# Kernel tuning notes

Measured on AMD Instinct MI355X. Metric: run time of the kernel, lower is better.

## Reference

```python
import jax, jax.numpy as jnp
import numpy as np

D = 7            # tree max depth (n_locations = 4**D = 16384)
M = 128          # memory_dim
N_KEYS = sum(4 ** i for i in range(1, D + 1))      # 21844
N_INTERNAL = N_KEYS // 4                           # 5461


def setup_inputs() -> dict:
    key = jax.random.key(0)
    ks = jax.random.split(key, 6)
    B, C = 4096, 64
    hidden = jax.random.normal(ks[0], (B, C), dtype=jnp.float32)
    Wq = jax.random.normal(ks[1], (M, C), dtype=jnp.float32) * 0.05
    bq = jnp.zeros((M,), dtype=jnp.float32)
    states = jax.random.normal(ks[2], (N_KEYS, M), dtype=jnp.float32)
    Wk = jax.random.normal(ks[3], (D, M, M), dtype=jnp.float32) * 0.05
    bk = jnp.zeros((D, M), dtype=jnp.float32)
    return {"hidden": hidden, "Wq": Wq, "bq": bq, "states": states, "Wk": Wk, "bk": bk}


def reference(hidden, Wq, bq, states, Wk, bk):
    B = hidden.shape[0]
    # hidden_to_query (pre-training path uses class_to_query): [B, M]
    query = hidden @ Wq.T + bq
    # make_keys: per-depth state_to_key linear + activation on batch-independent states
    keys = []
    cursor = 0
    for i in range(D):
        n = 4 ** (i + 1)
        keys.append(jax.nn.relu(states[cursor:cursor + n] @ Wk[i].T + bk[i]))
        cursor += n
    keys = jnp.concatenate(keys, axis=0)               # [N_KEYS, M]
    # compute_scores: bmm(keys, query^T) -> [B, N_INTERNAL, 4]
    scores = jnp.einsum('km,bm->bk', keys, query).reshape(B, N_INTERNAL, 4)
    # to_location_distribution (is_consistent, pre_training): cumulative log-softmax down the tree
    logp = jax.nn.log_softmax(scores, axis=-1)         # [B, N_INTERNAL, 4]
    dists = []
    cur = None
    cursor = 0
    for d in range(1, D + 1):
        n_parents = 4 ** (d - 1)
        layer = logp[:, cursor:cursor + n_parents, :].reshape(B, 4 ** d)
        cur = layer if cur is None else jnp.repeat(cur, 4, axis=-1) + layer
        dists.append(cur)                              # [B, 4**d]
        cursor += n_parents
    return tuple(dists)
```

## Files before the change

### kernel.cpp

```cpp
#include <hip/hip_runtime.h>
#include <hip/hip_bf16.h>
#include <math.h>

#define MDIM 128
#define CDIM 64
#define NTILES 1366

typedef __attribute__((ext_vector_type(8))) __bf16 bf16x8;
typedef __attribute__((ext_vector_type(4))) float f32x4;

__global__ __launch_bounds__(256) void k_cvtw(const float* __restrict__ Wk,
                                              __hip_bfloat16* __restrict__ wkb) {
  const int i = blockIdx.x * 256 + threadIdx.x;
  float4 v = *reinterpret_cast<const float4*>(Wk + (size_t)i * 4);
  __hip_bfloat16 h[4];
  h[0] = __float2bfloat16(v.x); h[1] = __float2bfloat16(v.y);
  h[2] = __float2bfloat16(v.z); h[3] = __float2bfloat16(v.w);
  unsigned long long bits;
  __builtin_memcpy(&bits, h, 8);
  *reinterpret_cast<unsigned long long*>(wkb + (size_t)i * 4) = bits;
}

#define STR 144

__global__ __launch_bounds__(64) void k_keys_mfma(const float* __restrict__ states,
                                                  const __hip_bfloat16* __restrict__ wkb,
                                                  const float* __restrict__ bk,
                                                  bf16x8* __restrict__ keysF) {
  __shared__ __align__(16) __hip_bfloat16 sT[16 * STR];
  const int lane = threadIdx.x;
  const int c = lane & 15, hi = lane >> 4;
  int blk = blockIdx.x, d, t;
  if      (blk < 2)   { d = blk; t = 0; }
  else if (blk < 6)   { d = 2; t = blk - 2; }
  else if (blk < 22)  { d = 3; t = blk - 6; }
  else if (blk < 86)  { d = 4; t = blk - 22; }
  else if (blk < 342) { d = 5; t = blk - 86; }
  else                { d = 6; t = blk - 342; }
  const int cumArr[7] = {0, 4, 20, 84, 340, 1364, 5460};
  const int k0 = cumArr[d] + 16 * t;

  bf16x8 sb[4];
  const float* srow = states + (size_t)(k0 + c) * MDIM;
#pragma unroll
  for (int kf = 0; kf < 4; ++kf) {
    float4 a = *reinterpret_cast<const float4*>(srow + kf * 32 + hi * 8);
    float4 b = *reinterpret_cast<const float4*>(srow + kf * 32 + hi * 8 + 4);
    bf16x8 v;
    v[0] = (__bf16)a.x; v[1] = (__bf16)a.y; v[2] = (__bf16)a.z; v[3] = (__bf16)a.w;
    v[4] = (__bf16)b.x; v[5] = (__bf16)b.y; v[6] = (__bf16)b.z; v[7] = (__bf16)b.w;
    sb[kf] = v;
  }

  const __hip_bfloat16* wkd = wkb + (size_t)d * MDIM * MDIM;
  const float* bkd = bk + d * MDIM;

#pragma unroll
  for (int ct = 0; ct < 8; ++ct) {
    bf16x8 aw[4];
    const __hip_bfloat16* wrow = wkd + (size_t)(ct * 16 + c) * MDIM;
#pragma unroll
    for (int kf = 0; kf < 4; ++kf)
      aw[kf] = *reinterpret_cast<const bf16x8*>(wrow + kf * 32 + hi * 8);
    f32x4 acc = {};
#pragma unroll
    for (int kf = 0; kf < 4; ++kf)
      acc = __builtin_amdgcn_mfma_f32_16x16x32_bf16(aw[kf], sb[kf], acc, 0, 0, 0);
    float4 bias = *reinterpret_cast<const float4*>(bkd + ct * 16 + hi * 4);
    __hip_bfloat16 hv[4];
    hv[0] = __float2bfloat16(fmaxf(acc[0] + bias.x, 0.f));
    hv[1] = __float2bfloat16(fmaxf(acc[1] + bias.y, 0.f));
    hv[2] = __float2bfloat16(fmaxf(acc[2] + bias.z, 0.f));
    hv[3] = __float2bfloat16(fmaxf(acc[3] + bias.w, 0.f));
    unsigned long long bits;
    __builtin_memcpy(&bits, hv, 8);
    *reinterpret_cast<unsigned long long*>(&sT[c * STR + ct * 16 + 4 * hi]) = bits;
  }

#pragma unroll
  for (int kf = 0; kf < 4; ++kf) {
    bf16x8 v = *reinterpret_cast<const bf16x8*>(&sT[c * STR + kf * 32 + hi * 8]);
    keysF[(size_t)(blk * 4 + kf) * 64 + lane] = v;
  }
}

__global__ __launch_bounds__(128) void k_query(const float* __restrict__ hidden,
                                               const float* __restrict__ Wq,
                                               const float* __restrict__ bq,
                                               __hip_bfloat16* __restrict__ query) {
  __shared__ __align__(16) float sH[4][CDIM];
  const int b0 = blockIdx.x * 4;
  const int m  = threadIdx.x;
  for (int idx = m; idx < 4 * CDIM; idx += 128)
    sH[idx >> 6][idx & 63] = hidden[(size_t)b0 * CDIM + idx];
  __syncthreads();
  const float4* wrow = (const float4*)(Wq + (size_t)m * CDIM);
  float acc0 = 0.f, acc1 = 0.f, acc2 = 0.f, acc3 = 0.f;
#pragma unroll
  for (int kq = 0; kq < CDIM / 4; ++kq) {
    float4 w = wrow[kq];
    float4 a = *(const float4*)&sH[0][kq * 4];
    float4 b = *(const float4*)&sH[1][kq * 4];
    float4 c = *(const float4*)&sH[2][kq * 4];
    float4 e = *(const float4*)&sH[3][kq * 4];
    acc0 += w.x * a.x + w.y * a.y + w.z * a.z + w.w * a.w;
    acc1 += w.x * b.x + w.y * b.y + w.z * b.z + w.w * b.w;
    acc2 += w.x * c.x + w.y * c.y + w.z * c.z + w.w * c.w;
    acc3 += w.x * e.x + w.y * e.y + w.z * e.z + w.w * e.w;
  }
  const float bias = bq[m];
  query[(size_t)(b0 + 0) * MDIM + m] = __float2bfloat16(acc0 + bias);
  query[(size_t)(b0 + 1) * MDIM + m] = __float2bfloat16(acc1 + bias);
  query[(size_t)(b0 + 2) * MDIM + m] = __float2bfloat16(acc2 + bias);
  query[(size_t)(b0 + 3) * MDIM + m] = __float2bfloat16(acc3 + bias);
}

#define D7STR 68

struct Frag { bf16x8 f[4]; };

__device__ __forceinline__ void load_frags(const bf16x8* __restrict__ kF,
                                           int blk, Frag& fr, int lane) {
#pragma unroll
  for (int kf = 0; kf < 4; ++kf)
    fr.f[kf] = kF[(size_t)(blk * 4 + kf) * 64 + lane];
}

__device__ __forceinline__ float gather_par(const f32x4 cp, int u, int lane) {
  const int src = u * 16 + (lane & 15);
  const float g0 = __shfl(cp[0], src, 64);
  const float g1 = __shfl(cp[1], src, 64);
  const float g2 = __shfl(cp[2], src, 64);
  const float g3 = __shfl(cp[3], src, 64);
  const int hi = lane >> 4;
  const float p01 = (hi & 1) ? g1 : g0;
  const float p23 = (hi & 1) ? g3 : g2;
  return (hi & 2) ? p23 : p01;
}

__device__ __forceinline__ void tile_step(
    const bf16x8* __restrict__ kF, const Frag& cur, int nextBlk, Frag& nxt,
    const bf16x8 (&qf)[4], const f32x4* cumPrev, int u, f32x4& cumOut,
    float* __restrict__ oPtr, size_t span, bool doStore, bool d1mask,
    float* __restrict__ d7dst, int lane) {
  const int c = lane & 15, hi = lane >> 4;

  if (nextBlk >= 0) load_frags(kF, nextBlk, nxt, lane);

  f32x4 acc = {};
  acc = __builtin_amdgcn_mfma_f32_16x16x32_bf16(cur.f[0], qf[0], acc, 0, 0, 0);
  acc = __builtin_amdgcn_mfma_f32_16x16x32_bf16(cur.f[1], qf[1], acc, 0, 0, 0);
  acc = __builtin_amdgcn_mfma_f32_16x16x32_bf16(cur.f[2], qf[2], acc, 0, 0, 0);
  acc = __builtin_amdgcn_mfma_f32_16x16x32_bf16(cur.f[3], qf[3], acc, 0, 0, 0);

  const float lse = __logf(__expf(acc[0]) + __expf(acc[1]) +
                           __expf(acc[2]) + __expf(acc[3]));
  float par = 0.f;
  if (cumPrev) par = gather_par(*cumPrev, u, lane);
  f32x4 cm;
  cm[0] = acc[0] - lse + par;
  cm[1] = acc[1] - lse + par;
  cm[2] = acc[2] - lse + par;
  cm[3] = acc[3] - lse + par;
  cumOut = cm;

  if (d7dst) {
    *reinterpret_cast<f32x4*>(d7dst + c * D7STR) = cm;
  } else if (doStore && (!d1mask || hi == 0)) {
    float4 o;
    o.x = cm[0]; o.y = cm[1]; o.z = cm[2]; o.w = cm[3];
    *reinterpret_cast<float4*>(oPtr + (size_t)c * span + hi * 4) = o;
  }
}

__global__ __launch_bounds__(256) void k_tree(const bf16x8* __restrict__ kF,
                                              const __hip_bfloat16* __restrict__ query,
                                              float* __restrict__ out, int B) {
  __shared__ __align__(16) float sD7[4][16 * D7STR];

  const int tid  = threadIdx.x;
  const int lane = tid & 63;
  const int w    = tid >> 6;
  const int c    = lane & 15, hi = lane >> 4;

  const int S5  = blockIdx.x & 63;
  const int bg  = blockIdx.x >> 6;
  const int T4  = S5 >> 2;
  const int T3  = S5 >> 4;
  const int b0w = bg * 64 + w * 16;

  float* d7w = &sD7[w][0];

  bf16x8 qf[4];
  {
    const __hip_bfloat16* qrow = query + (size_t)(b0w + c) * MDIM;
#pragma unroll
    for (int kf = 0; kf < 4; ++kf)
      qf[kf] = *reinterpret_cast<const bf16x8*>(qrow + kf * 32 + hi * 8);
  }

  Frag fA, fB;
  load_frags(kF, 0, fA, lane);

  f32x4 c1, c2, c3, c4, c5, c6, c7;

  tile_step(kF, fA, 1, fB, qf, nullptr, 0, c1,
            out + (size_t)b0w * 4, 4, S5 == 0, true, nullptr, lane);
  tile_step(kF, fB, 2 + T3, fA, qf, &c1, 0, c2,
            out + (size_t)4 * B + (size_t)b0w * 16, 16, S5 == 0, false,
            nullptr, lane);
  tile_step(kF, fA, 6 + T4, fB, qf, &c2, T3, c3,
            out + (size_t)20 * B + (size_t)b0w * 64 + 16 * T3, 64,
            (S5 & 15) == 0, false, nullptr, lane);
  tile_step(kF, fB, 22 + S5, fA, qf, &c3, T4 & 3, c4,
            out + (size_t)84 * B + (size_t)b0w * 256 + 16 * T4, 256,
            (S5 & 3) == 0, false, nullptr, lane);
  tile_step(kF, fA, 86 + 4 * S5, fB, qf, &c4, S5 & 3, c5,
            out + (size_t)340 * B + (size_t)b0w * 1024 + 16 * S5, 1024,
            true, false, nullptr, lane);

#pragma unroll
  for (int u5p = 0; u5p < 2; ++u5p) {
#pragma unroll
    for (int half = 0; half < 2; ++half) {
      const int u5 = u5p * 2 + half;
      Frag& f0 = (half == 0) ? fB : fA;
      Frag& f1 = (half == 0) ? fA : fB;
      const int T6 = 4 * S5 + u5;
      const int d7b = 342 + 16 * S5 + 4 * u5;
      tile_step(kF, f0, d7b, f1, qf, &c5, u5, c6,
                out + (size_t)1364 * B + (size_t)b0w * 4096 + 16 * T6, 4096,
                true, false, nullptr, lane);
      tile_step(kF, f1, d7b + 1, f0, qf, &c6, 0, c7,
                nullptr, 0, false, false, d7w + 0 * 16 + hi * 4, lane);
      tile_step(kF, f0, d7b + 2, f1, qf, &c6, 1, c7,
                nullptr, 0, false, false, d7w + 1 * 16 + hi * 4, lane);
      tile_step(kF, f1, d7b + 3, f0, qf, &c6, 2, c7,
                nullptr, 0, false, false, d7w + 2 * 16 + hi * 4, lane);
      tile_step(kF, f0, (u5 < 3) ? (86 + 4 * S5 + u5 + 1) : -1, f1, qf, &c6, 3, c7,
                nullptr, 0, false, false, d7w + 3 * 16 + hi * 4, lane);
      {
        float* dst = out + (size_t)5460 * B + (size_t)b0w * 16384 + 64 * T6;
#pragma unroll
        for (int j = 0; j < 4; ++j) {
          const int r = j * 4 + hi;
          f32x4 v = *reinterpret_cast<const f32x4*>(d7w + r * D7STR + c * 4);
          float4 o;
          o.x = v[0]; o.y = v[1]; o.z = v[2]; o.w = v[3];
          *reinterpret_cast<float4*>(dst + (size_t)r * 16384 + c * 4) = o;
        }
      }
    }
  }
}

extern "C" void kernel_launch(void* const* d_in, const int* in_sizes, int n_in,
                              void* d_out, int out_size, void* d_ws, size_t ws_size,
                              hipStream_t stream) {
  const float* hidden = (const float*)d_in[0];
  const float* Wq     = (const float*)d_in[1];
  const float* bq     = (const float*)d_in[2];
  const float* states = (const float*)d_in[3];
  const float* Wk     = (const float*)d_in[4];
  const float* bk     = (const float*)d_in[5];
  float* out = (float*)d_out;
  const int B = in_sizes[0] / CDIM;

  __hip_bfloat16* base  = (__hip_bfloat16*)d_ws;
  bf16x8* keysF = (bf16x8*)base;
  __hip_bfloat16* query = base + (size_t)NTILES * 4 * 64 * 8;
  __hip_bfloat16* wkb   = query + (size_t)B * MDIM;

  k_cvtw<<<(7 * MDIM * MDIM) / (256 * 4), 256, 0, stream>>>(Wk, wkb);
  k_query<<<B / 4, 128, 0, stream>>>(hidden, Wq, bq, query);
  k_keys_mfma<<<NTILES, 64, 0, stream>>>(states, wkb, bk, keysF);

  k_tree<<<(B / 64) * 64, 256, 0, stream>>>(keysF, query, out, B);
}
```

Measured before the change: 122.8 us.

## Process two 16-row batch tiles per wave to reuse key fragments

Each wave now handles 32 batch rows (two 16-row tiles) instead of 16, reusing every loaded key fragment for two sets of MFMAs. The grid is halved and the shared depth-7 staging buffer doubled. The aim is to halve key-fragment global loads and per-tile overhead per batch row, at the cost of more registers (two query fragment sets and two cumulative vectors per level), which may lower occupancy and gives fewer blocks to spread across CUs.

Measured after the change: 119.4 us. 2.7% less time.

```diff
diff --git a/kernel.cpp b/kernel.cpp
--- a/kernel.cpp
+++ b/kernel.cpp
@@ -140,43 +140,46 @@
 
 __device__ __forceinline__ void tile_step(
     const bf16x8* __restrict__ kF, const Frag& cur, int nextBlk, Frag& nxt,
-    const bf16x8 (&qf)[4], const f32x4* cumPrev, int u, f32x4& cumOut,
+    const bf16x8 (&qf)[2][4], const f32x4* cumPrev, int u, f32x4 (&cumOut)[2],
     float* __restrict__ oPtr, size_t span, bool doStore, bool d1mask,
     float* __restrict__ d7dst, int lane) {
   const int c = lane & 15, hi = lane >> 4;
 
   if (nextBlk >= 0) load_frags(kF, nextBlk, nxt, lane);
 
-  f32x4 acc = {};
-  acc = __builtin_amdgcn_mfma_f32_16x16x32_bf16(cur.f[0], qf[0], acc, 0, 0, 0);
-  acc = __builtin_amdgcn_mfma_f32_16x16x32_bf16(cur.f[1], qf[1], acc, 0, 0, 0);
-  acc = __builtin_amdgcn_mfma_f32_16x16x32_bf16(cur.f[2], qf[2], acc, 0, 0, 0);
-  acc = __builtin_amdgcn_mfma_f32_16x16x32_bf16(cur.f[3], qf[3], acc, 0, 0, 0);
-
-  const float lse = __logf(__expf(acc[0]) + __expf(acc[1]) +
-                           __expf(acc[2]) + __expf(acc[3]));
-  float par = 0.f;
-  if (cumPrev) par = gather_par(*cumPrev, u, lane);
-  f32x4 cm;
-  cm[0] = acc[0] - lse + par;
-  cm[1] = acc[1] - lse + par;
-  cm[2] = acc[2] - lse + par;
-  cm[3] = acc[3] - lse + par;
-  cumOut = cm;
-
-  if (d7dst) {
-    *reinterpret_cast<f32x4*>(d7dst + c * D7STR) = cm;
-  } else if (doStore && (!d1mask || hi == 0)) {
-    float4 o;
-    o.x = cm[0]; o.y = cm[1]; o.z = cm[2]; o.w = cm[3];
-    *reinterpret_cast<float4*>(oPtr + (size_t)c * span + hi * 4) = o;
+#pragma unroll
+  for (int bt = 0; bt < 2; ++bt) {
+    f32x4 acc = {};
+    acc = __builtin_amdgcn_mfma_f32_16x16x32_bf16(cur.f[0], qf[bt][0], acc, 0, 0, 0);
+    acc = __builtin_amdgcn_mfma_f32_16x16x32_bf16(cur.f[1], qf[bt][1], acc, 0, 0, 0);
+    acc = __builtin_amdgcn_mfma_f32_16x16x32_bf16(cur.f[2], qf[bt][2], acc, 0, 0, 0);
+    acc = __builtin_amdgcn_mfma_f32_16x16x32_bf16(cur.f[3], qf[bt][3], acc, 0, 0, 0);
+
+    const float lse = __logf(__expf(acc[0]) + __expf(acc[1]) +
+                             __expf(acc[2]) + __expf(acc[3]));
+    float par = 0.f;
+    if (cumPrev) par = gather_par(cumPrev[bt], u, lane);
+    f32x4 cm;
+    cm[0] = acc[0] - lse + par;
+    cm[1] = acc[1] - lse + par;
+    cm[2] = acc[2] - lse + par;
+    cm[3] = acc[3] - lse + par;
+    cumOut[bt] = cm;
+
+    if (d7dst) {
+      *reinterpret_cast<f32x4*>(d7dst + (bt * 16 + c) * D7STR) = cm;
+    } else if (doStore && (!d1mask || hi == 0)) {
+      float4 o;
+      o.x = cm[0]; o.y = cm[1]; o.z = cm[2]; o.w = cm[3];
+      *reinterpret_cast<float4*>(oPtr + (size_t)(bt * 16 + c) * span + hi * 4) = o;
+    }
   }
 }
 
 __global__ __launch_bounds__(256) void k_tree(const bf16x8* __restrict__ kF,
                                               const __hip_bfloat16* __restrict__ query,
                                               float* __restrict__ out, int B) {
-  __shared__ __align__(16) float sD7[4][16 * D7STR];
+  __shared__ __align__(16) float sD7[4][32 * D7STR];
 
   const int tid  = threadIdx.x;
   const int lane = tid & 63;
@@ -187,35 +190,36 @@
   const int bg  = blockIdx.x >> 6;
   const int T4  = S5 >> 2;
   const int T3  = S5 >> 4;
-  const int b0w = bg * 64 + w * 16;
+  const int b0w = bg * 128 + w * 32;
 
   float* d7w = &sD7[w][0];
 
-  bf16x8 qf[4];
-  {
-    const __hip_bfloat16* qrow = query + (size_t)(b0w + c) * MDIM;
+  bf16x8 qf[2][4];
+#pragma unroll
+  for (int bt = 0; bt < 2; ++bt) {
+    const __hip_bfloat16* qrow = query + (size_t)(b0w + bt * 16 + c) * MDIM;
 #pragma unroll
     for (int kf = 0; kf < 4; ++kf)
-      qf[kf] = *reinterpret_cast<const bf16x8*>(qrow + kf * 32 + hi * 8);
+      qf[bt][kf] = *reinterpret_cast<const bf16x8*>(qrow + kf * 32 + hi * 8);
   }
 
   Frag fA, fB;
   load_frags(kF, 0, fA, lane);
 
-  f32x4 c1, c2, c3, c4, c5, c6, c7;
+  f32x4 c1[2], c2[2], c3[2], c4[2], c5[2], c6[2], c7[2];
 
   tile_step(kF, fA, 1, fB, qf, nullptr, 0, c1,
             out + (size_t)b0w * 4, 4, S5 == 0, true, nullptr, lane);
-  tile_step(kF, fB, 2 + T3, fA, qf, &c1, 0, c2,
+  tile_step(kF, fB, 2 + T3, fA, qf, c1, 0, c2,
             out + (size_t)4 * B + (size_t)b0w * 16, 16, S5 == 0, false,
             nullptr, lane);
-  tile_step(kF, fA, 6 + T4, fB, qf, &c2, T3, c3,
+  tile_step(kF, fA, 6 + T4, fB, qf, c2, T3, c3,
             out + (size_t)20 * B + (size_t)b0w * 64 + 16 * T3, 64,
             (S5 & 15) == 0, false, nullptr, lane);
-  tile_step(kF, fB, 22 + S5, fA, qf, &c3, T4 & 3, c4,
+  tile_step(kF, fB, 22 + S5, fA, qf, c3, T4 & 3, c4,
             out + (size_t)84 * B + (size_t)b0w * 256 + 16 * T4, 256,
             (S5 & 3) == 0, false, nullptr, lane);
-  tile_step(kF, fA, 86 + 4 * S5, fB, qf, &c4, S5 & 3, c5,
+  tile_step(kF, fA, 86 + 4 * S5, fB, qf, c4, S5 & 3, c5,
             out + (size_t)340 * B + (size_t)b0w * 1024 + 16 * S5, 1024,
             true, false, nullptr, lane);
 
@@ -228,21 +232,21 @@
       Frag& f1 = (half == 0) ? fA : fB;
       const int T6 = 4 * S5 + u5;
       const int d7b = 342 + 16 * S5 + 4 * u5;
-      tile_step(kF, f0, d7b, f1, qf, &c5, u5, c6,
+      tile_step(kF, f0, d7b, f1, qf, c5, u5, c6,
                 out + (size_t)1364 * B + (size_t)b0w * 4096 + 16 * T6, 4096,
                 true, false, nullptr, lane);
-      tile_step(kF, f1, d7b + 1, f0, qf, &c6, 0, c7,
+      tile_step(kF, f1, d7b + 1, f0, qf, c6, 0, c7,
                 nullptr, 0, false, false, d7w + 0 * 16 + hi * 4, lane);
-      tile_step(kF, f0, d7b + 2, f1, qf, &c6, 1, c7,
+      tile_step(kF, f0, d7b + 2, f1, qf, c6, 1, c7,
                 nullptr, 0, false, false, d7w + 1 * 16 + hi * 4, lane);
-      tile_step(kF, f1, d7b + 3, f0, qf, &c6, 2, c7,
+      tile_step(kF, f1, d7b + 3, f0, qf, c6, 2, c7,
                 nullptr, 0, false, false, d7w + 2 * 16 + hi * 4, lane);
-      tile_step(kF, f0, (u5 < 3) ? (86 + 4 * S5 + u5 + 1) : -1, f1, qf, &c6, 3, c7,
+      tile_step(kF, f0, (u5 < 3) ? (86 + 4 * S5 + u5 + 1) : -1, f1, qf, c6, 3, c7,
                 nullptr, 0, false, false, d7w + 3 * 16 + hi * 4, lane);
       {
         float* dst = out + (size_t)5460 * B + (size_t)b0w * 16384 + 64 * T6;
 #pragma unroll
-        for (int j = 0; j < 4; ++j) {
+        for (int j = 0; j < 8; ++j) {
           const int r = j * 4 + hi;
           f32x4 v = *reinterpret_cast<const f32x4*>(d7w + r * D7STR + c * 4);
           float4 o;
@@ -275,5 +279,5 @@
   k_query<<<B / 4, 128, 0, stream>>>(hidden, Wq, bq, query);
   k_keys_mfma<<<NTILES, 64, 0, stream>>>(states, wkb, bk, keysF);
 
-  k_tree<<<(B / 64) * 64, 256, 0, stream>>>(keysF, query, out, B);
-}
+  k_tree<<<(B / 128) * 64, 256, 0, stream>>>(keysF, query, out, B);
+}
```
